# Kernel optimization log

Hardware: AMD Instinct MI355X
Metric: run time of the kernel (lower is better)

Reference implementation:

```python
import jax, jax.numpy as jnp
import numpy as np
from jax import lax

M1, M2 = 16, 16  # retained Fourier modes per spatial dim


def _spectral_conv(x, w1, w2):
    # x: [B, C, H, W] real; w1/w2: [C, C, M1, M2, 2] (re, im)
    B, C, H, W = x.shape
    xf = jnp.fft.rfft2(x, norm='ortho')            # [B, C, H, W//2+1] complex
    w1c = w1[..., 0] + 1j * w1[..., 1]
    w2c = w2[..., 0] + 1j * w2[..., 1]
    top = jnp.einsum('bixy,ioxy->boxy', xf[:, :, :M1, :M2], w1c)
    bot = jnp.einsum('bixy,ioxy->boxy', xf[:, :, -M1:, :M2], w2c)
    of = jnp.zeros((B, C, H, W // 2 + 1), dtype=xf.dtype)
    of = of.at[:, :, :M1, :M2].set(top).at[:, :, -M1:, :M2].set(bot)
    return jnp.fft.irfft2(of, s=(H, W), norm='ortho')


def _fno_block(x, w1, w2, skip_w):
    # spectral conv + linear (1x1 conv, no bias) skip
    return _spectral_conv(x, w1, w2) + jnp.einsum('bixy,io->boxy', x, skip_w)


def setup_inputs() -> dict:
    key = jax.random.key(0)
    ks = jax.random.split(key, 6)
    B, T, C, H, W = 4, 8, 64, 64, 64
    scale = 1.0 / (C * C)
    return {
        'x': jax.random.normal(ks[0], (B, T, C, H, W), dtype=jnp.float32),
        'sw1': jax.random.normal(ks[1], (6, C, C, M1, M2, 2), dtype=jnp.float32) * scale,
        'sw2': jax.random.normal(ks[2], (6, C, C, M1, M2, 2), dtype=jnp.float32) * scale,
        'skw': jax.random.normal(ks[3], (6, C, C), dtype=jnp.float32) * 0.02,
        'gate_b': jax.random.normal(ks[4], (3,), dtype=jnp.float32),
        'bias_h': jax.random.normal(ks[5], (1,), dtype=jnp.float32),
    }


def reference(x, sw1, sw2, skw, gate_b, bias_h):
    B, T, C, H, W = x.shape

    def f(i, inp):
        return _fno_block(inp, sw1[i], sw2[i], skw[i])

    def cell(xt, h):
        z = jax.nn.sigmoid(f(0, xt) + f(1, h) + gate_b[0])
        r = jax.nn.sigmoid(f(2, xt) + f(3, h) + gate_b[1])
        h_hat = jax.nn.selu(f(4, xt) + f(5, r * h) + gate_b[2])
        return (1.0 - z) * h + z * h_hat

    def step(h, xt):
        h = cell(xt, h)
        return h, None

    h0 = jnp.full((B, C, H, W), bias_h[0], dtype=x.dtype)
    h_final, _ = lax.scan(step, h0, jnp.moveaxis(x, 1, 0))  # scan over T
    return h_final  # return_sequences=False -> final hidden state [B, C, H, W]
```

## Files before the change

kernel.cpp:

```cpp
#include <hip/hip_runtime.h>

#define BB_ 4
#define TT_ 8
#define CC_ 64
#define HW 4096
#define UMAP 1024
#define STEP 0.09817477042468103f

#define OFF_UXALL 0
#define OFF_UH    (OFF_UXALL + TT_*256*UMAP)
#define OFF_URH   (OFF_UH + 256*UMAP)
#define OFF_SX    (OFF_URH + 256*UMAP)
#define OFF_SPART (OFF_SX + 3*TT_*256*UMAP)
#define OFF_H     (OFF_SPART + 2*8*256*UMAP)
#define OFF_Z     (OFF_H + BB_*CC_*HW)
#define OFF_RH    (OFF_Z + BB_*CC_*HW)
#define OFF_PH    (OFF_RH + BB_*CC_*HW)

__global__ __launch_bounds__(256) void k_init(float* __restrict__ hb,
                                              float* __restrict__ Uh,
                                              const float* __restrict__ bias_h) {
    float v = bias_h[0];
    int blk = blockIdx.x;
    if (blk < 1024) {
        int idx = (blk * 256 + threadIdx.x) * 4;
        *(float4*)(hb + idx) = make_float4(v, v, v, v);
    } else {
        int map = blk - 1024;
        float4 z = make_float4(0.f, 0.f, 0.f, 0.f);
        if (threadIdx.x == 0) z.x = 64.f * v;
        *(float4*)(Uh + (size_t)map * UMAP + threadIdx.x * 4) = z;
    }
}

__device__ __forceinline__ void dft_stages(const float* __restrict__ su,
                                           float* __restrict__ FxR, float* __restrict__ FxI,
                                           float* __restrict__ dst) {
    int tid = threadIdx.x;
    int kx = tid & 15, yb = tid >> 4;
    float stc, sts;
    __sincosf(-STEP * (float)kx, &sts, &stc);
    float wr = 1.f, wi = 0.f;
    float aR[4] = {0, 0, 0, 0}, aI[4] = {0, 0, 0, 0};
    for (int x = 0; x < 64; x++) {
        #pragma unroll
        for (int j = 0; j < 4; j++) {
            float v = su[(yb + 16 * j) * 65 + x];
            aR[j] = fmaf(v, wr, aR[j]);
            aI[j] = fmaf(v, wi, aI[j]);
        }
        float t = wr * stc - wi * sts;
        wi = wr * sts + wi * stc;
        wr = t;
    }
    #pragma unroll
    for (int j = 0; j < 4; j++) {
        FxR[(yb + 16 * j) * 16 + kx] = aR[j];
        FxI[(yb + 16 * j) * 16 + kx] = aI[j];
    }
    __syncthreads();
    int kb = tid >> 4;
    float c0, s0, c1, s1;
    __sincosf(-STEP * (float)kb, &s0, &c0);
    __sincosf(-STEP * (float)(kb + 48), &s1, &c1);
    float w0r = 1, w0i = 0, w1r = 1, w1i = 0;
    float A0r = 0, A0i = 0, A1r = 0, A1i = 0;
    for (int y = 0; y < 64; y++) {
        float Fr = FxR[y * 16 + kx], Fi = FxI[y * 16 + kx];
        A0r = fmaf(Fr, w0r, A0r); A0r = fmaf(-Fi, w0i, A0r);
        A0i = fmaf(Fr, w0i, A0i); A0i = fmaf(Fi, w0r, A0i);
        A1r = fmaf(Fr, w1r, A1r); A1r = fmaf(-Fi, w1i, A1r);
        A1i = fmaf(Fr, w1i, A1i); A1i = fmaf(Fi, w1r, A1i);
        float t0 = w0r * c0 - w0i * s0; w0i = w0r * s0 + w0i * c0; w0r = t0;
        float t1 = w1r * c1 - w1i * s1; w1i = w1r * s1 + w1i * c1; w1r = t1;
    }
    const float sc = 1.f / 64.f;
    float2* d2 = (float2*)dst;
    d2[kb * 16 + kx]        = make_float2(A0r * sc, A0i * sc);
    d2[(kb + 16) * 16 + kx] = make_float2(A1r * sc, A1i * sc);
}

__device__ __forceinline__ void dft_stages_512(const float* __restrict__ su,
                                               float* __restrict__ FxR, float* __restrict__ FxI,
                                               float* __restrict__ dst) {
    int tid = threadIdx.x;
    int kx = tid & 15, yb = tid >> 4;
    float stc, sts;
    __sincosf(-STEP * (float)kx, &sts, &stc);
    float wr = 1.f, wi = 0.f;
    float aR[2] = {0, 0}, aI[2] = {0, 0};
    for (int x = 0; x < 64; x++) {
        #pragma unroll
        for (int j = 0; j < 2; j++) {
            float v = su[(yb + 32 * j) * 65 + x];
            aR[j] = fmaf(v, wr, aR[j]);
            aI[j] = fmaf(v, wi, aI[j]);
        }
        float t = wr * stc - wi * sts;
        wi = wr * sts + wi * stc;
        wr = t;
    }
    #pragma unroll
    for (int j = 0; j < 2; j++) {
        FxR[(yb + 32 * j) * 16 + kx] = aR[j];
        FxI[(yb + 32 * j) * 16 + kx] = aI[j];
    }
    __syncthreads();
    int kb = tid >> 4;
    int ky = (kb < 16) ? kb : kb + 32;
    float c0, s0;
    __sincosf(-STEP * (float)ky, &s0, &c0);
    float w0r = 1, w0i = 0, A0r = 0, A0i = 0;
    for (int y = 0; y < 64; y++) {
        float Fr = FxR[y * 16 + kx], Fi = FxI[y * 16 + kx];
        A0r = fmaf(Fr, w0r, A0r); A0r = fmaf(-Fi, w0i, A0r);
        A0i = fmaf(Fr, w0i, A0i); A0i = fmaf(Fi, w0r, A0i);
        float t0 = w0r * c0 - w0i * s0; w0i = w0r * s0 + w0i * c0; w0r = t0;
    }
    const float sc = 1.f / 64.f;
    ((float2*)dst)[kb * 16 + kx] = make_float2(A0r * sc, A0i * sc);
}

__global__ __launch_bounds__(256) void k_dft_x(const float* __restrict__ x,
                                               float* __restrict__ Uxall) {
    __shared__ float su[64 * 65];
    __shared__ float FxR[1024], FxI[1024];
    int blk = blockIdx.x;
    int t = blk >> 8, map = blk & 255;
    int b = map >> 6, c = map & 63;
    const float* src = x + (((size_t)b * TT_ + t) * CC_ + c) * HW;
    int tid = threadIdx.x;
    #pragma unroll
    for (int k = 0; k < 4; k++) {
        int off = k * 1024 + tid * 4;
        float4 v = *(const float4*)(src + off);
        int y = off >> 6, xx = off & 63;
        su[y * 65 + xx + 0] = v.x; su[y * 65 + xx + 1] = v.y;
        su[y * 65 + xx + 2] = v.z; su[y * 65 + xx + 3] = v.w;
    }
    __syncthreads();
    dft_stages(su, FxR, FxI, Uxall + ((size_t)t * 256 + map) * UMAP);
}

__device__ __forceinline__ void mix_load(const float2* __restrict__ W2,
                                         const float2* __restrict__ U2, int i,
                                         float2 w[4], float2 u[4]) {
    const float2* wp = W2 + (size_t)i * 16384;
    const float2* up = U2 + (size_t)i * 512;
    w[0] = wp[0]; w[1] = wp[256]; w[2] = wp[512]; w[3] = wp[768];
    u[0] = up[0]; u[1] = up[32768]; u[2] = up[65536]; u[3] = up[98304];
}

__device__ __forceinline__ void mix_fma(const float2 w[4], const float2 u[4],
                                        float aR[4][4], float aI[4][4]) {
    #pragma unroll
    for (int oo = 0; oo < 4; oo++)
        #pragma unroll
        for (int bb = 0; bb < 4; bb++) {
            aR[oo][bb] = fmaf(u[bb].x, w[oo].x, aR[oo][bb]);
            aR[oo][bb] = fmaf(-u[bb].y, w[oo].y, aR[oo][bb]);
            aI[oo][bb] = fmaf(u[bb].x, w[oo].y, aI[oo][bb]);
            aI[oo][bb] = fmaf(u[bb].y, w[oo].x, aI[oo][bb]);
        }
}

__device__ __forceinline__ void mix_accum(const float2* __restrict__ W2,
                                          const float2* __restrict__ U2,
                                          int niter, float aR[4][4], float aI[4][4])
{
    float2 wA[4], uA[4], wB[4], uB[4], wN[4], uN[4];
    mix_load(W2, U2, 0, wA, uA);
    mix_load(W2, U2, 1, wB, uB);
    for (int i = 0; i + 2 < niter; i += 2) {
        mix_load(W2, U2, i + 2, wN, uN);
        mix_fma(wA, uA, aR, aI);
        #pragma unroll
        for (int k = 0; k < 4; k++) { wA[k] = wN[k]; uA[k] = uN[k]; }
        mix_load(W2, U2, i + 3, wN, uN);
        mix_fma(wB, uB, aR, aI);
        #pragma unroll
        for (int k = 0; k < 4; k++) { wB[k] = wN[k]; uB[k] = uN[k]; }
    }
    mix_fma(wA, uA, aR, aI);
    mix_fma(wB, uB, aR, aI);
}

__global__ __launch_bounds__(256, 4) void k_mix_x(
    const float* __restrict__ Uxall,
    const float* __restrict__ sw1, const float* __restrict__ sw2,
    float* __restrict__ Sx)
{
    __shared__ float4 Wt4[2][256];
    __shared__ float4 Ut4[2][1024];
    int blk = blockIdx.x;
    int mq = blk & 15;
    int op = (blk >> 4) & 7;
    int half = (blk >> 7) & 1;
    int li = blk >> 8;
    int l = li * 2;
    int tid = threadIdx.x;
    int m0 = mq * 16;
    int o0 = op * 8;
    const float2* wsrc = (const float2*)(half ? sw2 : sw1);
    const float2* usrc = (const float2*)Uxall;

    int wl = tid & 7;
    int wrow = tid >> 3;
    int wii = wrow >> 3, woo = wrow & 7;
    const float4* wg4 = (const float4*)(wsrc
        + (((size_t)(l * 64 + wii) * 64) + o0 + woo) * 256 + m0) + wl;
    int ut_ = wrow >> 2, ub_ = wrow & 3;
    const float4* ug4 = (const float4*)(usrc
        + (size_t)ut_ * 131072 + (size_t)ub_ * 32768 + half * 256 + m0) + wl;

    int mt = tid & 15, pp = tid >> 4;
    float aR[8][2], aI[8][2];
    #pragma unroll
    for (int oo = 0; oo < 8; oo++) {
        aR[oo][0] = 0.f; aR[oo][1] = 0.f;
        aI[oo][0] = 0.f; aI[oo][1] = 0.f;
    }

    float4 wv  = wg4[0];
    float4 uv0 = ug4[0];
    float4 uv1 = ug4[256];
    float4 uv2 = ug4[512];
    float4 uv3 = ug4[768];

    for (int c = 0; c < 16; ++c) {
        int cb = c & 1;
        Wt4[cb][tid] = wv;
        Ut4[cb][tid] = uv0;
        Ut4[cb][256 + tid] = uv1;
        Ut4[cb][512 + tid] = uv2;
        Ut4[cb][768 + tid] = uv3;
        if (c < 15) {
            size_t ib = (size_t)(c + 1) * 4;
            wv  = wg4[ib * 8192];
            uv0 = ug4[ib * 256];
            uv1 = ug4[(ib + 1) * 256];
            uv2 = ug4[(ib + 2) * 256];
            uv3 = ug4[(ib + 3) * 256];
        }
        __syncthreads();
        const float2* Wl = (const float2*)Wt4[cb];
        const float2* Ul = (const float2*)Ut4[cb];
        #pragma unroll
        for (int ii = 0; ii < 4; ii++) {
            float2 u0 = Ul[(ii * 32 + 2 * pp) * 16 + mt];
            float2 u1 = Ul[(ii * 32 + 2 * pp + 1) * 16 + mt];
            #pragma unroll
            for (int oo = 0; oo < 8; oo++) {
                float2 w = Wl[(ii * 8 + oo) * 16 + mt];
                aR[oo][0] = fmaf(u0.x, w.x, aR[oo][0]);
                aR[oo][0] = fmaf(-u0.y, w.y, aR[oo][0]);
                aI[oo][0] = fmaf(u0.x, w.y, aI[oo][0]);
                aI[oo][0] = fmaf(u0.y, w.x, aI[oo][0]);
                aR[oo][1] = fmaf(u1.x, w.x, aR[oo][1]);
                aR[oo][1] = fmaf(-u1.y, w.y, aR[oo][1]);
                aI[oo][1] = fmaf(u1.x, w.y, aI[oo][1]);
                aI[oo][1] = fmaf(u1.y, w.x, aI[oo][1]);
            }
        }
        __syncthreads();
    }

    float2* S2 = (float2*)Sx;
    #pragma unroll
    for (int oo = 0; oo < 8; oo++)
        #pragma unroll
        for (int j = 0; j < 2; j++) {
            int tb = 2 * pp + j;
            int t = tb >> 2, b = tb & 3;
            S2[((size_t)(li * 8 + t) * 256 + b * 64 + o0 + oo) * 512
               + half * 256 + m0 + mt] = make_float2(aR[oo][j], aI[oo][j]);
        }
}

__device__ __forceinline__ void mix_body_h(int blk, int l0, int l1,
    const float* __restrict__ U,
    const float* __restrict__ sw1, const float* __restrict__ sw2,
    float* __restrict__ Spart)
{
    int og = blk & 15;
    int ic = (blk >> 4) & 7;
    int half = (blk >> 7) & 1;
    int g = (blk >> 8) & 1;
    int m = threadIdx.x;
    int o0 = og * 4, ib = ic * 8;
    int l = g ? l1 : l0;
    const float2* wt = (const float2*)(half ? sw2 : sw1);
    const float2* W2 = wt + (((size_t)l * 64 + ib) * 64 + o0) * 256 + m;
    const float2* U2 = (const float2*)U + (size_t)ib * 512 + half * 256 + m;
    float aR[4][4], aI[4][4];
    #pragma unroll
    for (int oo = 0; oo < 4; oo++)
        #pragma unroll
        for (int b = 0; b < 4; b++) { aR[oo][b] = 0.f; aI[oo][b] = 0.f; }
    mix_accum(W2, U2, 8, aR, aI);
    float2* S2 = (float2*)Spart;
    #pragma unroll
    for (int oo = 0; oo < 4; oo++)
        #pragma unroll
        for (int b = 0; b < 4; b++)
            S2[((size_t)(g * 8 + ic) * 256 + b * 64 + o0 + oo) * 512 + half * 256 + m]
                = make_float2(aR[oo][b], aI[oo][b]);
}

__device__ __forceinline__ void fma16(const float4 w, const float4 u, float acc[4][4]) {
    acc[0][0] = fmaf(u.x, w.x, acc[0][0]); acc[0][1] = fmaf(u.y, w.x, acc[0][1]);
    acc[0][2] = fmaf(u.z, w.x, acc[0][2]); acc[0][3] = fmaf(u.w, w.x, acc[0][3]);
    acc[1][0] = fmaf(u.x, w.y, acc[1][0]); acc[1][1] = fmaf(u.y, w.y, acc[1][1]);
    acc[1][2] = fmaf(u.z, w.y, acc[1][2]); acc[1][3] = fmaf(u.w, w.y, acc[1][3]);
    acc[2][0] = fmaf(u.x, w.z, acc[2][0]); acc[2][1] = fmaf(u.y, w.z, acc[2][1]);
    acc[2][2] = fmaf(u.z, w.z, acc[2][2]); acc[2][3] = fmaf(u.w, w.z, acc[2][3]);
    acc[3][0] = fmaf(u.x, w.w, acc[3][0]); acc[3][1] = fmaf(u.y, w.w, acc[3][1]);
    acc[3][2] = fmaf(u.z, w.w, acc[3][2]); acc[3][3] = fmaf(u.w, w.w, acc[3][3]);
}

__device__ __forceinline__ void skip_gemm(int rr, float* __restrict__ sW,
    const float* __restrict__ uA, long long bsA,
    const float* __restrict__ uB, long long bsB,
    const float* __restrict__ skw, int lA, int lB, float gb,
    float* __restrict__ out)
{
    int pxc = rr & 31, oh = (rr >> 5) & 1, b = rr >> 6;
    int tid = threadIdx.x;
    int ot = tid & 7, pt = tid >> 3;
    #pragma unroll
    for (int n = 0; n < 4; n++) {
        int idx = n * 1024 + tid * 4;
        int k = idx >> 5, oc = idx & 31;
        int p = k >> 6, i = k & 63;
        *(float4*)(sW + idx) =
            *(const float4*)(skw + (p ? lB : lA) * 4096 + i * 64 + oh * 32 + oc);
    }
    __syncthreads();
    float acc[4][4];
    #pragma unroll
    for (int oo = 0; oo < 4; oo++)
        #pragma unroll
        for (int q = 0; q < 4; q++) acc[oo][q] = 0.f;
    const float* pa = uA + (long long)b * bsA + pxc * 128 + pt * 4;
    const float* pb = uB + (long long)b * bsB + pxc * 128 + pt * 4;
    const float4* sW4 = (const float4*)sW;
    #pragma unroll 4
    for (int i = 0; i < 64; i++) {
        float4 ua = *(const float4*)(pa + (size_t)i * HW);
        float4 wa = sW4[i * 8 + ot];
        fma16(wa, ua, acc);
        float4 ub = *(const float4*)(pb + (size_t)i * HW);
        float4 wb = sW4[(64 + i) * 8 + ot];
        fma16(wb, ub, acc);
    }
    float* op = out + ((long long)(b * 64 + oh * 32 + ot * 4)) * HW + pxc * 128 + pt * 4;
    #pragma unroll
    for (int oo = 0; oo < 4; oo++) {
        float4 r = make_float4(acc[oo][0] + gb, acc[oo][1] + gb,
                               acc[oo][2] + gb, acc[oo][3] + gb);
        *(float4*)(op + (size_t)oo * HW) = r;
    }
}

__global__ __launch_bounds__(256) void k_front_zr(
    const float* __restrict__ Uh,
    const float* __restrict__ xt, const float* __restrict__ hb,
    const float* __restrict__ sw1, const float* __restrict__ sw2,
    const float* __restrict__ skw, const float* __restrict__ gate_b,
    float* __restrict__ Spart, float* __restrict__ zb, float* __restrict__ rhb)
{
    __shared__ float smem[4096];
    int blk = blockIdx.x;
    if (blk < 512) {
        mix_body_h(blk, 1, 3, Uh, sw1, sw2, Spart);
    } else {
        int r = blk - 512;
        int g = r >> 8;
        skip_gemm(r & 255, smem,
                  xt, (long long)TT_ * CC_ * HW, hb, (long long)CC_ * HW,
                  skw, g ? 2 : 0, g ? 3 : 1, gate_b[g], g ? rhb : zb);
    }
}

__global__ __launch_bounds__(256) void k_front_h(
    const float* __restrict__ Urh,
    const float* __restrict__ xt, const float* __restrict__ rhb,
    const float* __restrict__ sw1, const float* __restrict__ sw2,
    const float* __restrict__ skw, const float* __restrict__ gate_b,
    float* __restrict__ Spart, float* __restrict__ phb)
{
    __shared__ float smem[4096];
    int blk = blockIdx.x;
    if (blk < 256) {
        mix_body_h(blk, 5, 5, Urh, sw1, sw2, Spart);
    } else {
        int r = blk - 256;
        skip_gemm(r, smem,
                  xt, (long long)TT_ * CC_ * HW, rhb, (long long)CC_ * HW,
                  skw, 4, 5, gate_b[2], phb);
    }
}

__device__ __forceinline__ void idft_stage1_512(const float* __restrict__ SR,
                                                const float* __restrict__ SI,
                                                float* __restrict__ GR, float* __restrict__ GI)
{
    int tid = threadIdx.x;
    int kx = tid & 15, yb = tid >> 4;
    #pragma unroll
    for (int j = 0; j < 2; j++) {
        int y = yb + 32 * j;
        float stc, sts;
        __sincosf(STEP * (float)y, &sts, &stc);
        float ar = 0.f, ai = 0.f;
        float wr = 1.f, wi = 0.f;
        for (int k = 0; k < 16; k++) {
            float sr_ = SR[k * 16 + kx], si_ = SI[k * 16 + kx];
            ar = fmaf(sr_, wr, ar); ar = fmaf(-si_, wi, ar);
            ai = fmaf(sr_, wi, ai); ai = fmaf(si_, wr, ai);
            float t = wr * stc - wi * sts; wi = wr * sts + wi * stc; wr = t;
        }
        int q = (3 * y) & 3;
        float w2r = (q == 0) ? 1.f : ((q == 2) ? -1.f : 0.f);
        float w2i = (q == 1) ? 1.f : ((q == 3) ? -1.f : 0.f);
        for (int k = 16; k < 32; k++) {
            float sr_ = SR[k * 16 + kx], si_ = SI[k * 16 + kx];
            ar = fmaf(sr_, w2r, ar); ar = fmaf(-si_, w2i, ar);
            ai = fmaf(sr_, w2i, ai); ai = fmaf(si_, w2r, ai);
            float t = w2r * stc - w2i * sts; w2i = w2r * sts + w2i * stc; w2r = t;
        }
        GR[y * 16 + kx] = ar;
        GI[y * 16 + kx] = ai;
    }
}

__global__ __launch_bounds__(512) void k_back_zr(
    const float* __restrict__ Spart, const float* __restrict__ Sx, int t,
    float* __restrict__ zb, float* __restrict__ rhb,
    const float* __restrict__ hb, float* __restrict__ Urh)
{
    __shared__ float smem[6208];
    float* SR = smem;
    float* SI = smem + 512;
    float* GR = smem + 1024;
    float* GI = smem + 2048;
    int g = blockIdx.x >> 8;
    int map = blockIdx.x & 255;
    int tid = threadIdx.x;
    {
        float2 v = ((const float2*)Sx)[((size_t)(g * 8 + t) * 256 + map) * 512 + tid];
        float sr = v.x, si = v.y;
        const float2* base = (const float2*)Spart;
        #pragma unroll
        for (int ic = 0; ic < 8; ic++) {
            float2 p = base[((size_t)(g * 8 + ic) * 256 + map) * 512 + tid];
            sr += p.x; si += p.y;
        }
        SR[tid] = sr; SI[tid] = si;
    }
    __syncthreads();
    idft_stage1_512(SR, SI, GR, GI);
    __syncthreads();
    int x = tid & 63, ybase = tid >> 6;
    float cx, sx;
    __sincosf(STEP * (float)x, &sx, &cx);
    size_t mo = (size_t)map * HW;
    float rhv[8];
    #pragma unroll
    for (int j = 0; j < 8; j++) {
        int y = ybase + 8 * j;
        float acc = GR[y * 16];
        float wr = cx, wi = sx;
        #pragma unroll
        for (int k = 1; k < 16; k++) {
            acc = fmaf(2.f * GR[y * 16 + k], wr, acc);
            acc = fmaf(-2.f * GI[y * 16 + k], wi, acc);
            float t2 = wr * cx - wi * sx; wi = wr * sx + wi * cx; wr = t2;
        }
        float val = acc * (1.f / 64.f);
        int idx = y * 64 + x;
        if (g == 0) {
            float pre = val + zb[mo + idx];
            zb[mo + idx] = 1.f / (1.f + __expf(-pre));
        } else {
            float pre = val + rhb[mo + idx];
            float rr = 1.f / (1.f + __expf(-pre));
            float rh = rr * hb[mo + idx];
            rhb[mo + idx] = rh;
            rhv[j] = rh;
        }
    }
    if (g == 0) return;
    __syncthreads();
    float* su = smem;
    #pragma unroll
    for (int j = 0; j < 8; j++) {
        int y = ybase + 8 * j;
        su[y * 65 + x] = rhv[j];
    }
    __syncthreads();
    dft_stages_512(su, smem + 4160, smem + 5184, Urh + (size_t)map * UMAP);
}

__global__ __launch_bounds__(512) void k_back_h(
    const float* __restrict__ Spart, const float* __restrict__ Sx, int t,
    const float* __restrict__ zb, const float* __restrict__ phb,
    float* __restrict__ hb, float* __restrict__ Uh)
{
    __shared__ float smem[6208];
    float* SR = smem;
    float* SI = smem + 512;
    float* GR = smem + 1024;
    float* GI = smem + 2048;
    int map = blockIdx.x & 255;
    int tid = threadIdx.x;
    {
        float2 v = ((const float2*)Sx)[((size_t)(2 * 8 + t) * 256 + map) * 512 + tid];
        float sr = v.x, si = v.y;
        const float2* base = (const float2*)Spart;
        #pragma unroll
        for (int ic = 0; ic < 8; ic++) {
            float2 p = base[((size_t)ic * 256 + map) * 512 + tid];
            sr += p.x; si += p.y;
        }
        SR[tid] = sr; SI[tid] = si;
    }
    __syncthreads();
    idft_stage1_512(SR, SI, GR, GI);
    __syncthreads();
    int x = tid & 63, ybase = tid >> 6;
    float cx, sx;
    __sincosf(STEP * (float)x, &sx, &cx);
    size_t mo = (size_t)map * HW;
    float hv[8];
    #pragma unroll
    for (int j = 0; j < 8; j++) {
        int y = ybase + 8 * j;
        float acc = GR[y * 16];
        float wr = cx, wi = sx;
        #pragma unroll
        for (int k = 1; k < 16; k++) {
            acc = fmaf(2.f * GR[y * 16 + k], wr, acc);
            acc = fmaf(-2.f * GI[y * 16 + k], wi, acc);
            float t2 = wr * cx - wi * sx; wi = wr * sx + wi * cx; wr = t2;
        }
        float val = acc * (1.f / 64.f);
        int idx = y * 64 + x;
        float pre = val + phb[mo + idx];
        float hh = (pre > 0.f) ? 1.0507009873554805f * pre
                               : 1.7580993408473766f * (__expf(pre) - 1.f);
        float z = zb[mo + idx];
        float hn = fmaf(z, hh - hb[mo + idx], hb[mo + idx]);
        hb[mo + idx] = hn;
        hv[j] = hn;
    }
    __syncthreads();
    float* su = smem;
    #pragma unroll
    for (int j = 0; j < 8; j++) {
        int y = ybase + 8 * j;
        su[y * 65 + x] = hv[j];
    }
    __syncthreads();
    dft_stages_512(su, smem + 4160, smem + 5184, Uh + (size_t)map * UMAP);
}

extern "C" void kernel_launch(void* const* d_in, const int* in_sizes, int n_in,
                              void* d_out, int out_size, void* d_ws, size_t ws_size,
                              hipStream_t stream)
{
    (void)in_sizes; (void)n_in; (void)out_size; (void)ws_size;
    const float* x   = (const float*)d_in[0];
    const float* sw1 = (const float*)d_in[1];
    const float* sw2 = (const float*)d_in[2];
    const float* skw = (const float*)d_in[3];
    const float* gb  = (const float*)d_in[4];
    const float* bh  = (const float*)d_in[5];
    float* ws    = (float*)d_ws;
    float* Uxall = ws + OFF_UXALL;
    float* Uh    = ws + OFF_UH;
    float* Urh   = ws + OFF_URH;
    float* Sx    = ws + OFF_SX;
    float* Sp    = ws + OFF_SPART;
    float* hb    = ws + OFF_H;
    float* zb    = ws + OFF_Z;
    float* rhb   = ws + OFF_RH;
    float* phb   = ws + OFF_PH;

    k_init<<<1280, 256, 0, stream>>>(hb, Uh, bh);
    k_dft_x<<<2048, 256, 0, stream>>>(x, Uxall);
    k_mix_x<<<768, 256, 0, stream>>>(Uxall, sw1, sw2, Sx);
    for (int t = 0; t < TT_; t++) {
        const float* xt = x + (size_t)t * CC_ * HW;
        k_front_zr<<<1024, 256, 0, stream>>>(Uh, xt, hb, sw1, sw2, skw, gb,
                                             Sp, zb, rhb);
        k_back_zr<<<512, 512, 0, stream>>>(Sp, Sx, t, zb, rhb, hb, Urh);
        k_front_h<<<512, 256, 0, stream>>>(Urh, xt, rhb, sw1, sw2, skw, gb,
                                           Sp, phb);
        k_back_h<<<256, 512, 0, stream>>>(Sp, Sx, t, zb, phb, hb, Uh);
    }
    hipMemcpyAsync(d_out, hb, (size_t)BB_ * CC_ * HW * sizeof(float),
                   hipMemcpyDeviceToDevice, stream);
}
```

Measured before the change: 748.4 us.

## Move z-gate finalize into h-front kernel and restructure x-mode mixing loads

The z-gate inverse-DFT and sigmoid finalize moves out of k_back_zr into extra blocks of k_front_h. It runs there alongside the h-gate spectral mixing and skip GEMM, so k_back_zr only handles the r gate. The h partial sums now go to a separate Spart slot so they do not collide with the z partials read in the same launch. Separately, k_mix_x now reads U values straight from global into registers and stores weights transposed in LDS for wide float4 reads, which removes one barrier per chunk. The cost is a heavier, less uniform k_front_h launch and uncoalesced float2 global loads for U.

```diff
diff --git a/kernel.cpp b/kernel.cpp
--- a/kernel.cpp
+++ b/kernel.cpp
@@ -190,8 +190,7 @@
     const float* __restrict__ sw1, const float* __restrict__ sw2,
     float* __restrict__ Sx)
 {
-    __shared__ float4 Wt4[2][256];
-    __shared__ float4 Ut4[2][1024];
+    __shared__ __align__(16) float2 Wl[2][640];
     int blk = blockIdx.x;
     int mq = blk & 15;
     int op = (blk >> 4) & 7;
@@ -209,11 +208,14 @@
     int wii = wrow >> 3, woo = wrow & 7;
     const float4* wg4 = (const float4*)(wsrc
         + (((size_t)(l * 64 + wii) * 64) + o0 + woo) * 256 + m0) + wl;
-    int ut_ = wrow >> 2, ub_ = wrow & 3;
-    const float4* ug4 = (const float4*)(usrc
-        + (size_t)ut_ * 131072 + (size_t)ub_ * 32768 + half * 256 + m0) + wl;
 
     int mt = tid & 15, pp = tid >> 4;
+    int tb0 = 2 * pp, tb1 = 2 * pp + 1;
+    const float2* up0 = usrc + (size_t)(tb0 >> 2) * 131072
+                        + (size_t)(tb0 & 3) * 32768 + half * 256 + m0 + mt;
+    const float2* up1 = usrc + (size_t)(tb1 >> 2) * 131072
+                        + (size_t)(tb1 & 3) * 32768 + half * 256 + m0 + mt;
+
     float aR[8][2], aI[8][2];
     #pragma unroll
     for (int oo = 0; oo < 8; oo++) {
@@ -221,37 +223,41 @@
         aI[oo][0] = 0.f; aI[oo][1] = 0.f;
     }
 
-    float4 wv  = wg4[0];
-    float4 uv0 = ug4[0];
-    float4 uv1 = ug4[256];
-    float4 uv2 = ug4[512];
-    float4 uv3 = ug4[768];
+    float4 wv = wg4[0];
+    Wl[0][(wii * 16 + 2 * wl) * 10 + woo]     = make_float2(wv.x, wv.y);
+    Wl[0][(wii * 16 + 2 * wl + 1) * 10 + woo] = make_float2(wv.z, wv.w);
+    wv = wg4[32768];
+    __syncthreads();
 
     for (int c = 0; c < 16; ++c) {
         int cb = c & 1;
-        Wt4[cb][tid] = wv;
-        Ut4[cb][tid] = uv0;
-        Ut4[cb][256 + tid] = uv1;
-        Ut4[cb][512 + tid] = uv2;
-        Ut4[cb][768 + tid] = uv3;
+        float2 u0v[4], u1v[4];
+        #pragma unroll
+        for (int ii = 0; ii < 4; ii++) {
+            u0v[ii] = up0[(size_t)(4 * c + ii) * 512];
+            u1v[ii] = up1[(size_t)(4 * c + ii) * 512];
+        }
         if (c < 15) {
-            size_t ib = (size_t)(c + 1) * 4;
-            wv  = wg4[ib * 8192];
-            uv0 = ug4[ib * 256];
-            uv1 = ug4[(ib + 1) * 256];
-            uv2 = ug4[(ib + 2) * 256];
-            uv3 = ug4[(ib + 3) * 256];
-        }
-        __syncthreads();
-        const float2* Wl = (const float2*)Wt4[cb];
-        const float2* Ul = (const float2*)Ut4[cb];
+            Wl[cb ^ 1][(wii * 16 + 2 * wl) * 10 + woo]     = make_float2(wv.x, wv.y);
+            Wl[cb ^ 1][(wii * 16 + 2 * wl + 1) * 10 + woo] = make_float2(wv.z, wv.w);
+            if (c < 14) wv = wg4[(size_t)(c + 2) * 32768];
+        }
         #pragma unroll
         for (int ii = 0; ii < 4; ii++) {
-            float2 u0 = Ul[(ii * 32 + 2 * pp) * 16 + mt];
-            float2 u1 = Ul[(ii * 32 + 2 * pp + 1) * 16 + mt];
+            const float2* wrow2 = &Wl[cb][(ii * 16 + mt) * 10];
+            float4 wq0 = *(const float4*)(wrow2 + 0);
+            float4 wq1 = *(const float4*)(wrow2 + 2);
+            float4 wq2 = *(const float4*)(wrow2 + 4);
+            float4 wq3 = *(const float4*)(wrow2 + 6);
+            float2 u0 = u0v[ii], u1 = u1v[ii];
+            float2 wz[8];
+            wz[0] = make_float2(wq0.x, wq0.y); wz[1] = make_float2(wq0.z, wq0.w);
+            wz[2] = make_float2(wq1.x, wq1.y); wz[3] = make_float2(wq1.z, wq1.w);
+            wz[4] = make_float2(wq2.x, wq2.y); wz[5] = make_float2(wq2.z, wq2.w);
+            wz[6] = make_float2(wq3.x, wq3.y); wz[7] = make_float2(wq3.z, wq3.w);
             #pragma unroll
             for (int oo = 0; oo < 8; oo++) {
-                float2 w = Wl[(ii * 8 + oo) * 16 + mt];
+                float2 w = wz[oo];
                 aR[oo][0] = fmaf(u0.x, w.x, aR[oo][0]);
                 aR[oo][0] = fmaf(-u0.y, w.y, aR[oo][0]);
                 aI[oo][0] = fmaf(u0.x, w.y, aI[oo][0]);
@@ -362,6 +368,85 @@
     }
 }
 
+__device__ __forceinline__ void idft_stage1_256(const float* __restrict__ SR,
+                                                const float* __restrict__ SI,
+                                                float* __restrict__ GR, float* __restrict__ GI)
+{
+    int tid = threadIdx.x;
+    int kx = tid & 15, yb = tid >> 4;
+    #pragma unroll
+    for (int j = 0; j < 4; j++) {
+        int y = yb + 16 * j;
+        float stc, sts;
+        __sincosf(STEP * (float)y, &sts, &stc);
+        float ar = 0.f, ai = 0.f;
+        float wr = 1.f, wi = 0.f;
+        for (int k = 0; k < 16; k++) {
+            float sr_ = SR[k * 16 + kx], si_ = SI[k * 16 + kx];
+            ar = fmaf(sr_, wr, ar); ar = fmaf(-si_, wi, ar);
+            ai = fmaf(sr_, wi, ai); ai = fmaf(si_, wr, ai);
+            float t = wr * stc - wi * sts; wi = wr * sts + wi * stc; wr = t;
+        }
+        int q = (3 * y) & 3;
+        float w2r = (q == 0) ? 1.f : ((q == 2) ? -1.f : 0.f);
+        float w2i = (q == 1) ? 1.f : ((q == 3) ? -1.f : 0.f);
+        for (int k = 16; k < 32; k++) {
+            float sr_ = SR[k * 16 + kx], si_ = SI[k * 16 + kx];
+            ar = fmaf(sr_, w2r, ar); ar = fmaf(-si_, w2i, ar);
+            ai = fmaf(sr_, w2i, ai); ai = fmaf(si_, w2r, ai);
+            float t = w2r * stc - w2i * sts; w2i = w2r * sts + w2i * stc; w2r = t;
+        }
+        GR[y * 16 + kx] = ar;
+        GI[y * 16 + kx] = ai;
+    }
+}
+
+__device__ __forceinline__ void z_finalize(int map, int t,
+    const float* __restrict__ Spart, const float* __restrict__ Sx,
+    float* __restrict__ zb, float* __restrict__ smem)
+{
+    float* SR = smem;
+    float* SI = smem + 512;
+    float* GR = smem + 1024;
+    float* GI = smem + 2048;
+    int tid = threadIdx.x;
+    {
+        float4 v = ((const float4*)Sx)[((size_t)t * 256 + map) * 256 + tid];
+        float sxr = v.x, sxi = v.y, syr = v.z, syi = v.w;
+        const float4* base = (const float4*)Spart;
+        #pragma unroll
+        for (int ic = 0; ic < 8; ic++) {
+            float4 p = base[((size_t)ic * 256 + map) * 256 + tid];
+            sxr += p.x; sxi += p.y; syr += p.z; syi += p.w;
+        }
+        SR[2 * tid] = sxr; SI[2 * tid] = sxi;
+        SR[2 * tid + 1] = syr; SI[2 * tid + 1] = syi;
+    }
+    __syncthreads();
+    idft_stage1_256(SR, SI, GR, GI);
+    __syncthreads();
+    int x = tid & 63, ybase = tid >> 6;
+    float cx, sx;
+    __sincosf(STEP * (float)x, &sx, &cx);
+    size_t mo = (size_t)map * HW;
+    #pragma unroll
+    for (int j = 0; j < 16; j++) {
+        int y = ybase + 4 * j;
+        float acc = GR[y * 16];
+        float wr = cx, wi = sx;
+        #pragma unroll
+        for (int k = 1; k < 16; k++) {
+            acc = fmaf(2.f * GR[y * 16 + k], wr, acc);
+            acc = fmaf(-2.f * GI[y * 16 + k], wi, acc);
+            float t2 = wr * cx - wi * sx; wi = wr * sx + wi * cx; wr = t2;
+        }
+        float val = acc * (1.f / 64.f);
+        int idx = y * 64 + x;
+        float pre = val + zb[mo + idx];
+        zb[mo + idx] = 1.f / (1.f + __expf(-pre));
+    }
+}
+
 __global__ __launch_bounds__(256) void k_front_zr(
     const float* __restrict__ Uh,
     const float* __restrict__ xt, const float* __restrict__ hb,
@@ -387,14 +472,17 @@
     const float* __restrict__ xt, const float* __restrict__ rhb,
     const float* __restrict__ sw1, const float* __restrict__ sw2,
     const float* __restrict__ skw, const float* __restrict__ gate_b,
-    float* __restrict__ Spart, float* __restrict__ phb)
+    float* __restrict__ Spart, float* __restrict__ phb,
+    const float* __restrict__ Sx, int t, float* __restrict__ zb)
 {
     __shared__ float smem[4096];
     int blk = blockIdx.x;
     if (blk < 256) {
+        z_finalize(blk, t, Spart, Sx, zb, smem);
+    } else if (blk < 512) {
         mix_body_h(blk, 5, 5, Urh, sw1, sw2, Spart);
     } else {
-        int r = blk - 256;
+        int r = blk - 512;
         skip_gemm(r, smem,
                   xt, (long long)TT_ * CC_ * HW, rhb, (long long)CC_ * HW,
                   skw, 4, 5, gate_b[2], phb);
@@ -436,7 +524,7 @@
 
 __global__ __launch_bounds__(512) void k_back_zr(
     const float* __restrict__ Spart, const float* __restrict__ Sx, int t,
-    float* __restrict__ zb, float* __restrict__ rhb,
+    float* __restrict__ rhb,
     const float* __restrict__ hb, float* __restrict__ Urh)
 {
     __shared__ float smem[6208];
@@ -444,16 +532,15 @@
     float* SI = smem + 512;
     float* GR = smem + 1024;
     float* GI = smem + 2048;
-    int g = blockIdx.x >> 8;
-    int map = blockIdx.x & 255;
+    int map = blockIdx.x;
     int tid = threadIdx.x;
     {
-        float2 v = ((const float2*)Sx)[((size_t)(g * 8 + t) * 256 + map) * 512 + tid];
+        float2 v = ((const float2*)Sx)[((size_t)(8 + t) * 256 + map) * 512 + tid];
         float sr = v.x, si = v.y;
         const float2* base = (const float2*)Spart;
         #pragma unroll
         for (int ic = 0; ic < 8; ic++) {
-            float2 p = base[((size_t)(g * 8 + ic) * 256 + map) * 512 + tid];
+            float2 p = base[((size_t)(8 + ic) * 256 + map) * 512 + tid];
             sr += p.x; si += p.y;
         }
         SR[tid] = sr; SI[tid] = si;
@@ -479,18 +566,12 @@
         }
         float val = acc * (1.f / 64.f);
         int idx = y * 64 + x;
-        if (g == 0) {
-            float pre = val + zb[mo + idx];
-            zb[mo + idx] = 1.f / (1.f + __expf(-pre));
-        } else {
-            float pre = val + rhb[mo + idx];
-            float rr = 1.f / (1.f + __expf(-pre));
-            float rh = rr * hb[mo + idx];
-            rhb[mo + idx] = rh;
-            rhv[j] = rh;
-        }
-    }
-    if (g == 0) return;
+        float pre = val + rhb[mo + idx];
+        float rr = 1.f / (1.f + __expf(-pre));
+        float rh = rr * hb[mo + idx];
+        rhb[mo + idx] = rh;
+        rhv[j] = rh;
+    }
     __syncthreads();
     float* su = smem;
     #pragma unroll
@@ -520,7 +601,7 @@
         const float2* base = (const float2*)Spart;
         #pragma unroll
         for (int ic = 0; ic < 8; ic++) {
-            float2 p = base[((size_t)ic * 256 + map) * 512 + tid];
+            float2 p = base[((size_t)(8 + ic) * 256 + map) * 512 + tid];
             sr += p.x; si += p.y;
         }
         SR[tid] = sr; SI[tid] = si;
@@ -594,9 +675,9 @@
         const float* xt = x + (size_t)t * CC_ * HW;
         k_front_zr<<<1024, 256, 0, stream>>>(Uh, xt, hb, sw1, sw2, skw, gb,
                                              Sp, zb, rhb);
-        k_back_zr<<<512, 512, 0, stream>>>(Sp, Sx, t, zb, rhb, hb, Urh);
-        k_front_h<<<512, 256, 0, stream>>>(Urh, xt, rhb, sw1, sw2, skw, gb,
-                                           Sp, phb);
+        k_back_zr<<<256, 512, 0, stream>>>(Sp, Sx, t, rhb, hb, Urh);
+        k_front_h<<<768, 256, 0, stream>>>(Urh, xt, rhb, sw1, sw2, skw, gb,
+                                           Sp, phb, Sx, t, zb);
         k_back_h<<<256, 512, 0, stream>>>(Sp, Sx, t, zb, phb, hb, Uh);
     }
     hipMemcpyAsync(d_out, hb, (size_t)BB_ * CC_ * HW * sizeof(float),
```

New measurement: 741.9 us. Within noise of the previous version (-0.9%).

## Fuse hidden-state spectral mixing into gate kernels, drop partial-sum buffer

Applied to the files above, without the earlier changes.

The per-step spectral channel mixing for the hidden-state terms moves out of the front kernels and into the gate/back kernels. Each thread now does the full 64-input-channel complex dot product for one output map and mode, instead of reading 8 partial sums from a workspace buffer. This removes the partial-sum writes and reads and leaves the front kernels as pure skip GEMMs. In exchange, each thread only accumulates one output, so weight and activation reuse across outputs and batches is lost. That raises global/L2 load traffic, and the mixing now sits on the serial critical path inside the smaller gate grids.

```diff
diff --git a/kernel.cpp b/kernel.cpp
--- a/kernel.cpp
+++ b/kernel.cpp
@@ -140,49 +140,6 @@
     }
     __syncthreads();
     dft_stages(su, FxR, FxI, Uxall + ((size_t)t * 256 + map) * UMAP);
-}
-
-__device__ __forceinline__ void mix_load(const float2* __restrict__ W2,
-                                         const float2* __restrict__ U2, int i,
-                                         float2 w[4], float2 u[4]) {
-    const float2* wp = W2 + (size_t)i * 16384;
-    const float2* up = U2 + (size_t)i * 512;
-    w[0] = wp[0]; w[1] = wp[256]; w[2] = wp[512]; w[3] = wp[768];
-    u[0] = up[0]; u[1] = up[32768]; u[2] = up[65536]; u[3] = up[98304];
-}
-
-__device__ __forceinline__ void mix_fma(const float2 w[4], const float2 u[4],
-                                        float aR[4][4], float aI[4][4]) {
-    #pragma unroll
-    for (int oo = 0; oo < 4; oo++)
-        #pragma unroll
-        for (int bb = 0; bb < 4; bb++) {
-            aR[oo][bb] = fmaf(u[bb].x, w[oo].x, aR[oo][bb]);
-            aR[oo][bb] = fmaf(-u[bb].y, w[oo].y, aR[oo][bb]);
-            aI[oo][bb] = fmaf(u[bb].x, w[oo].y, aI[oo][bb]);
-            aI[oo][bb] = fmaf(u[bb].y, w[oo].x, aI[oo][bb]);
-        }
-}
-
-__device__ __forceinline__ void mix_accum(const float2* __restrict__ W2,
-                                          const float2* __restrict__ U2,
-                                          int niter, float aR[4][4], float aI[4][4])
-{
-    float2 wA[4], uA[4], wB[4], uB[4], wN[4], uN[4];
-    mix_load(W2, U2, 0, wA, uA);
-    mix_load(W2, U2, 1, wB, uB);
-    for (int i = 0; i + 2 < niter; i += 2) {
-        mix_load(W2, U2, i + 2, wN, uN);
-        mix_fma(wA, uA, aR, aI);
-        #pragma unroll
-        for (int k = 0; k < 4; k++) { wA[k] = wN[k]; uA[k] = uN[k]; }
-        mix_load(W2, U2, i + 3, wN, uN);
-        mix_fma(wB, uB, aR, aI);
-        #pragma unroll
-        for (int k = 0; k < 4; k++) { wB[k] = wN[k]; uB[k] = uN[k]; }
-    }
-    mix_fma(wA, uA, aR, aI);
-    mix_fma(wB, uB, aR, aI);
 }
 
 __global__ __launch_bounds__(256, 4) void k_mix_x(
@@ -277,36 +234,6 @@
         }
 }
 
-__device__ __forceinline__ void mix_body_h(int blk, int l0, int l1,
-    const float* __restrict__ U,
-    const float* __restrict__ sw1, const float* __restrict__ sw2,
-    float* __restrict__ Spart)
-{
-    int og = blk & 15;
-    int ic = (blk >> 4) & 7;
-    int half = (blk >> 7) & 1;
-    int g = (blk >> 8) & 1;
-    int m = threadIdx.x;
-    int o0 = og * 4, ib = ic * 8;
-    int l = g ? l1 : l0;
-    const float2* wt = (const float2*)(half ? sw2 : sw1);
-    const float2* W2 = wt + (((size_t)l * 64 + ib) * 64 + o0) * 256 + m;
-    const float2* U2 = (const float2*)U + (size_t)ib * 512 + half * 256 + m;
-    float aR[4][4], aI[4][4];
-    #pragma unroll
-    for (int oo = 0; oo < 4; oo++)
-        #pragma unroll
-        for (int b = 0; b < 4; b++) { aR[oo][b] = 0.f; aI[oo][b] = 0.f; }
-    mix_accum(W2, U2, 8, aR, aI);
-    float2* S2 = (float2*)Spart;
-    #pragma unroll
-    for (int oo = 0; oo < 4; oo++)
-        #pragma unroll
-        for (int b = 0; b < 4; b++)
-            S2[((size_t)(g * 8 + ic) * 256 + b * 64 + o0 + oo) * 512 + half * 256 + m]
-                = make_float2(aR[oo][b], aI[oo][b]);
-}
-
 __device__ __forceinline__ void fma16(const float4 w, const float4 u, float acc[4][4]) {
     acc[0][0] = fmaf(u.x, w.x, acc[0][0]); acc[0][1] = fmaf(u.y, w.x, acc[0][1]);
     acc[0][2] = fmaf(u.z, w.x, acc[0][2]); acc[0][3] = fmaf(u.w, w.x, acc[0][3]);
@@ -362,43 +289,28 @@
     }
 }
 
-__global__ __launch_bounds__(256) void k_front_zr(
-    const float* __restrict__ Uh,
+__global__ __launch_bounds__(256) void k_skip_zr(
     const float* __restrict__ xt, const float* __restrict__ hb,
-    const float* __restrict__ sw1, const float* __restrict__ sw2,
     const float* __restrict__ skw, const float* __restrict__ gate_b,
-    float* __restrict__ Spart, float* __restrict__ zb, float* __restrict__ rhb)
+    float* __restrict__ zb, float* __restrict__ rhb)
 {
     __shared__ float smem[4096];
     int blk = blockIdx.x;
-    if (blk < 512) {
-        mix_body_h(blk, 1, 3, Uh, sw1, sw2, Spart);
-    } else {
-        int r = blk - 512;
-        int g = r >> 8;
-        skip_gemm(r & 255, smem,
-                  xt, (long long)TT_ * CC_ * HW, hb, (long long)CC_ * HW,
-                  skw, g ? 2 : 0, g ? 3 : 1, gate_b[g], g ? rhb : zb);
-    }
-}
-
-__global__ __launch_bounds__(256) void k_front_h(
-    const float* __restrict__ Urh,
+    int g = blk >> 8;
+    skip_gemm(blk & 255, smem,
+              xt, (long long)TT_ * CC_ * HW, hb, (long long)CC_ * HW,
+              skw, g ? 2 : 0, g ? 3 : 1, gate_b[g], g ? rhb : zb);
+}
+
+__global__ __launch_bounds__(256) void k_skip_h(
     const float* __restrict__ xt, const float* __restrict__ rhb,
-    const float* __restrict__ sw1, const float* __restrict__ sw2,
     const float* __restrict__ skw, const float* __restrict__ gate_b,
-    float* __restrict__ Spart, float* __restrict__ phb)
+    float* __restrict__ phb)
 {
     __shared__ float smem[4096];
-    int blk = blockIdx.x;
-    if (blk < 256) {
-        mix_body_h(blk, 5, 5, Urh, sw1, sw2, Spart);
-    } else {
-        int r = blk - 256;
-        skip_gemm(r, smem,
-                  xt, (long long)TT_ * CC_ * HW, rhb, (long long)CC_ * HW,
-                  skw, 4, 5, gate_b[2], phb);
-    }
+    skip_gemm(blockIdx.x, smem,
+              xt, (long long)TT_ * CC_ * HW, rhb, (long long)CC_ * HW,
+              skw, 4, 5, gate_b[2], phb);
 }
 
 __device__ __forceinline__ void idft_stage1_512(const float* __restrict__ SR,
@@ -434,8 +346,33 @@
     }
 }
 
-__global__ __launch_bounds__(512) void k_back_zr(
-    const float* __restrict__ Spart, const float* __restrict__ Sx, int t,
+__device__ __forceinline__ void gate_mix(int l, int b, int o, int half, int m,
+    const float* __restrict__ U,
+    const float* __restrict__ sw1, const float* __restrict__ sw2,
+    float& sr, float& si)
+{
+    const float2* wp = (const float2*)(half ? sw2 : sw1)
+                       + ((size_t)l * 64 * 64 + o) * 256 + m;
+    const float2* up = (const float2*)U + (size_t)b * 64 * 512 + half * 256 + m;
+    sr = 0.f; si = 0.f;
+    for (int i = 0; i < 64; i += 8) {
+        float2 w[8], u[8];
+        #pragma unroll
+        for (int k = 0; k < 8; k++) {
+            w[k] = wp[(size_t)(i + k) * 16384];
+            u[k] = up[(size_t)(i + k) * 512];
+        }
+        #pragma unroll
+        for (int k = 0; k < 8; k++) {
+            sr = fmaf(u[k].x, w[k].x, sr); sr = fmaf(-u[k].y, w[k].y, sr);
+            si = fmaf(u[k].x, w[k].y, si); si = fmaf(u[k].y, w[k].x, si);
+        }
+    }
+}
+
+__global__ __launch_bounds__(512) void k_gate_zr(
+    const float* __restrict__ Uh, const float* __restrict__ Sx, int t,
+    const float* __restrict__ sw1, const float* __restrict__ sw2,
     float* __restrict__ zb, float* __restrict__ rhb,
     const float* __restrict__ hb, float* __restrict__ Urh)
 {
@@ -446,17 +383,15 @@
     float* GI = smem + 2048;
     int g = blockIdx.x >> 8;
     int map = blockIdx.x & 255;
-    int tid = threadIdx.x;
+    int b = map >> 6, o = map & 63;
+    int tid = threadIdx.x;
+    int half = tid >> 8, m = tid & 255;
     {
+        float sr, si;
+        gate_mix(2 * g + 1, b, o, half, m, Uh, sw1, sw2, sr, si);
         float2 v = ((const float2*)Sx)[((size_t)(g * 8 + t) * 256 + map) * 512 + tid];
-        float sr = v.x, si = v.y;
-        const float2* base = (const float2*)Spart;
-        #pragma unroll
-        for (int ic = 0; ic < 8; ic++) {
-            float2 p = base[((size_t)(g * 8 + ic) * 256 + map) * 512 + tid];
-            sr += p.x; si += p.y;
-        }
-        SR[tid] = sr; SI[tid] = si;
+        SR[tid] = sr + v.x;
+        SI[tid] = si + v.y;
     }
     __syncthreads();
     idft_stage1_512(SR, SI, GR, GI);
@@ -502,8 +437,9 @@
     dft_stages_512(su, smem + 4160, smem + 5184, Urh + (size_t)map * UMAP);
 }
 
-__global__ __launch_bounds__(512) void k_back_h(
-    const float* __restrict__ Spart, const float* __restrict__ Sx, int t,
+__global__ __launch_bounds__(512) void k_gate_h(
+    const float* __restrict__ Urh, const float* __restrict__ Sx, int t,
+    const float* __restrict__ sw1, const float* __restrict__ sw2,
     const float* __restrict__ zb, const float* __restrict__ phb,
     float* __restrict__ hb, float* __restrict__ Uh)
 {
@@ -513,17 +449,15 @@
     float* GR = smem + 1024;
     float* GI = smem + 2048;
     int map = blockIdx.x & 255;
-    int tid = threadIdx.x;
+    int b = map >> 6, o = map & 63;
+    int tid = threadIdx.x;
+    int half = tid >> 8, m = tid & 255;
     {
+        float sr, si;
+        gate_mix(5, b, o, half, m, Urh, sw1, sw2, sr, si);
         float2 v = ((const float2*)Sx)[((size_t)(2 * 8 + t) * 256 + map) * 512 + tid];
-        float sr = v.x, si = v.y;
-        const float2* base = (const float2*)Spart;
-        #pragma unroll
-        for (int ic = 0; ic < 8; ic++) {
-            float2 p = base[((size_t)ic * 256 + map) * 512 + tid];
-            sr += p.x; si += p.y;
-        }
-        SR[tid] = sr; SI[tid] = si;
+        SR[tid] = sr + v.x;
+        SI[tid] = si + v.y;
     }
     __syncthreads();
     idft_stage1_512(SR, SI, GR, GI);
@@ -581,7 +515,6 @@
     float* Uh    = ws + OFF_UH;
     float* Urh   = ws + OFF_URH;
     float* Sx    = ws + OFF_SX;
-    float* Sp    = ws + OFF_SPART;
     float* hb    = ws + OFF_H;
     float* zb    = ws + OFF_Z;
     float* rhb   = ws + OFF_RH;
@@ -592,12 +525,10 @@
     k_mix_x<<<768, 256, 0, stream>>>(Uxall, sw1, sw2, Sx);
     for (int t = 0; t < TT_; t++) {
         const float* xt = x + (size_t)t * CC_ * HW;
-        k_front_zr<<<1024, 256, 0, stream>>>(Uh, xt, hb, sw1, sw2, skw, gb,
-                                             Sp, zb, rhb);
-        k_back_zr<<<512, 512, 0, stream>>>(Sp, Sx, t, zb, rhb, hb, Urh);
-        k_front_h<<<512, 256, 0, stream>>>(Urh, xt, rhb, sw1, sw2, skw, gb,
-                                           Sp, phb);
-        k_back_h<<<256, 512, 0, stream>>>(Sp, Sx, t, zb, phb, hb, Uh);
+        k_skip_zr<<<512, 256, 0, stream>>>(xt, hb, skw, gb, zb, rhb);
+        k_gate_zr<<<512, 512, 0, stream>>>(Uh, Sx, t, sw1, sw2, zb, rhb, hb, Urh);
+        k_skip_h<<<256, 256, 0, stream>>>(xt, rhb, skw, gb, phb);
+        k_gate_h<<<256, 512, 0, stream>>>(Urh, Sx, t, sw1, sw2, zb, phb, hb, Uh);
     }
     hipMemcpyAsync(d_out, hb, (size_t)BB_ * CC_ * HW * sizeof(float),
                    hipMemcpyDeviceToDevice, stream);
```

Result: slower. 854.2 us (+14.1%).
